# Kernel tuning notes

Measured on AMD Instinct MI355X. Metric: run time of the kernel, lower is better.

The kernel has to match this reference:

```python
import jax, jax.numpy as jnp
import numpy as np

QS = (0.25, 0.5, 0.75)


def _pool(inputs, maskb):
    """Masked summary-stats pooling: [B,S,F] -> [B, 7F+1]."""
    B, S, F = inputs.shape
    m = maskb[:, :, None].astype(inputs.dtype)          # [B,S,1]
    count = jnp.sum(m, axis=1)                          # [B,1]
    safe = jnp.maximum(count, 1.0)
    is_empty = count == 0                               # [B,1]
    mean = jnp.sum(inputs * m, axis=1) / safe           # [B,F]
    diffs = (inputs - mean[:, None, :]) * m
    var = jnp.sum(diffs * diffs, axis=1) / jnp.maximum(safe - 1.0, 1.0)
    std = jnp.sqrt(var)
    pinf = jnp.asarray(jnp.inf, inputs.dtype)
    mb3 = maskb[:, :, None]
    minv = jnp.min(jnp.where(mb3, inputs, pinf), axis=1)
    maxv = jnp.max(jnp.where(mb3, inputs, -pinf), axis=1)
    # nanquantile: sort with invalid entries pushed to the end (+inf),
    # then linear interpolation at q*(n-1) over the first n valid entries.
    xs = jnp.sort(jnp.where(mb3, inputs, pinf), axis=1)  # [B,S,F]
    n1 = jnp.maximum(count[:, 0] - 1.0, 0.0)             # [B]
    qv = []
    for q in QS:
        pos = q * n1                                     # [B]
        lo = jnp.clip(jnp.floor(pos).astype(jnp.int32), 0, S - 1)
        hi = jnp.clip(jnp.ceil(pos).astype(jnp.int32), 0, S - 1)
        frac = (pos - lo.astype(inputs.dtype))[:, None]  # [B,1]
        lov = jnp.take_along_axis(xs, jnp.broadcast_to(lo[:, None, None], (B, 1, F)), axis=1)[:, 0]
        hiv = jnp.take_along_axis(xs, jnp.broadcast_to(hi[:, None, None], (B, 1, F)), axis=1)[:, 0]
        qv.append(lov * (1.0 - frac) + hiv * frac)
    stats = [count, mean, qv[1], minv, maxv, std, qv[0], qv[2]]
    stats = [jnp.where(is_empty, jnp.zeros_like(s), s) for s in stats]
    return jnp.concatenate(stats, axis=1)                # [B, 7F+1]


def setup_inputs() -> dict:
    key = jax.random.key(0)
    ks = jax.random.split(key, 8)
    B, S, F = 256, 16384, 16
    D = 7 * F + 1  # 113
    inputs = jax.random.normal(ks[0], (B, S, F), dtype=jnp.float32)
    mask = jax.random.randint(ks[1], (B, S), 0, 2) > 0
    W1 = jax.random.normal(ks[2], (D, 16), dtype=jnp.float32) * 0.05
    b1 = jnp.zeros((16,), jnp.float32)
    W2 = jax.random.normal(ks[3], (16, 4), dtype=jnp.float32) * 0.05
    b2 = jnp.zeros((4,), jnp.float32)
    W3 = jax.random.normal(ks[4], (4, 1), dtype=jnp.float32) * 0.05
    b3 = jnp.zeros((1,), jnp.float32)
    return {"inputs": inputs, "mask": mask, "W1": W1, "b1": b1,
            "W2": W2, "b2": b2, "W3": W3, "b3": b3}


def reference(inputs, mask, W1, b1, W2, b2, W3, b3):
    pooled = _pool(inputs, mask)
    h = jax.nn.relu(pooled @ W1 + b1)   # dropout is identity in eval mode
    h = jax.nn.relu(h @ W2 + b2)
    return h @ W3 + b3                  # [B,1]
```

## Files before the change

### kernel.cpp

```cpp
#include <hip/hip_runtime.h>
#include <stdint.h>

#define B_DIM 256
#define S_DIM 16384
#define HALF_S 8192
#define D_DIM 113
#define NTH 1024
#define NIT 32
#define HDW 1024

__device__ __forceinline__ uint32_t enc_key(float v) {
    uint32_t u = __float_as_uint(v);
    uint32_t m = (uint32_t)((int32_t)u >> 31) | 0x80000000u;
    return u ^ m;
}
__device__ __forceinline__ float dec_key(uint32_t k) {
    uint32_t u = (k & 0x80000000u) ? (k ^ 0x80000000u) : ~k;
    return __uint_as_float(u);
}
__device__ __forceinline__ uint32_t umn(uint32_t a, uint32_t b) { return a < b ? a : b; }
__device__ __forceinline__ uint32_t umx(uint32_t a, uint32_t b) { return a > b ? a : b; }

__global__ __launch_bounds__(NTH, 8) void hist_kernel(
        const float* __restrict__ in, const unsigned char* __restrict__ mb,
        uint32_t* __restrict__ hws, float* __restrict__ psum,
        float* __restrict__ pssq, uint32_t* __restrict__ pkmin,
        uint32_t* __restrict__ pkmax, uint32_t* __restrict__ pn) {
    __shared__ uint32_t uni[16384];
    __shared__ float w_sum[16][16], w_ssq[16][16];
    __shared__ uint32_t w_kmin[16][16], w_kmax[16][16], w_cnt[16];
    __shared__ uint32_t s_det;

    const int t = threadIdx.x;
    const int b = blockIdx.x & 255;
    const int sh = blockIdx.x >> 8;
    const int c = t & 3;
    const float INFV = __uint_as_float(0x7F800000u);

    #pragma unroll
    for (int i = 0; i < 16; ++i) uni[i * NTH + t] = 0u;
    if (t == 0) s_det = 0u;
    {
        const uint32_t* mw32 = reinterpret_cast<const uint32_t*>(mb);
        uint32_t x = mw32[b * 1024 + t] & 0xFFFFFF00u;
        unsigned long long any = __ballot(x != 0);
        if ((t & 63) == 0 && any) atomicOr(&s_det, 1u);
    }
    __syncthreads();
    const size_t mstride = s_det ? (size_t)1 : (size_t)4;
    const unsigned char* __restrict__ mrow = mb + (size_t)b * S_DIM * mstride;

    const float4* __restrict__ base4 = reinterpret_cast<const float4*>(in)
        + (size_t)b * S_DIM * 4;

    float sumv[4] = {0.f, 0.f, 0.f, 0.f}, ssqv[4] = {0.f, 0.f, 0.f, 0.f};
    uint32_t kmn[4] = {~0u, ~0u, ~0u, ~0u}, kmx[4] = {0u, 0u, 0u, 0u};
    uint32_t cnt = 0;
    #pragma unroll 4
    for (int i = 0; i < NIT; ++i) {
        int s = sh * HALF_S + i * 256 + (t >> 2);
        float4 v = base4[(size_t)s * 4 + c];
        uint32_t m = mrow[(size_t)s * mstride] ? 1u : 0u;
        cnt += (c == 0) ? m : 0u;
        float vv[4] = {v.x, v.y, v.z, v.w};
        #pragma unroll
        for (int q = 0; q < 4; ++q) {
            float vh = m ? vv[q] : INFV;
            uint32_t key = enc_key(vh);
            kmn[q] = umn(kmn[q], key);
            kmx[q] = umx(kmx[q], m ? key : 0u);
            float vs = m ? vv[q] : 0.f;
            sumv[q] += vs;
            ssqv[q] = fmaf(vs, vs, ssqv[q]);
            if (m) {
                uint32_t bin = key >> 21;
                atomicAdd(&uni[((uint32_t)c * 4 + q) * HDW + (bin >> 1)],
                          (bin & 1) ? 65536u : 1u);
            }
        }
    }

    #pragma unroll
    for (int off = 32; off >= 4; off >>= 1) {
        #pragma unroll
        for (int q = 0; q < 4; ++q) {
            sumv[q] += __shfl_down(sumv[q], off);
            ssqv[q] += __shfl_down(ssqv[q], off);
            kmn[q] = umn(kmn[q], __shfl_down(kmn[q], off));
            kmx[q] = umx(kmx[q], __shfl_down(kmx[q], off));
        }
        cnt += __shfl_down(cnt, off);
    }
    {
        int w = t >> 6, lane = t & 63;
        if (lane < 4) {
            #pragma unroll
            for (int q = 0; q < 4; ++q) {
                w_sum[w][lane * 4 + q] = sumv[q];
                w_ssq[w][lane * 4 + q] = ssqv[q];
                w_kmin[w][lane * 4 + q] = kmn[q];
                w_kmax[w][lane * 4 + q] = kmx[q];
            }
            if (lane == 0) w_cnt[w] = cnt;
        }
    }
    __syncthreads();

    if (t < 16) {
        float s0 = 0.f, q0 = 0.f;
        uint32_t mnv = ~0u, mxv = 0u;
        for (int w = 0; w < 16; ++w) {
            s0 += w_sum[w][t]; q0 += w_ssq[w][t];
            mnv = umn(mnv, w_kmin[w][t]); mxv = umx(mxv, w_kmax[w][t]);
        }
        int bid = blockIdx.x;
        psum[bid * 16 + t] = s0; pssq[bid * 16 + t] = q0;
        pkmin[bid * 16 + t] = mnv; pkmax[bid * 16 + t] = mxv;
        if (t == 0) {
            uint32_t nn = 0;
            for (int w = 0; w < 16; ++w) nn += w_cnt[w];
            pn[bid] = nn;
        }
    }
    uint32_t* hb = hws + (size_t)blockIdx.x * 16384;
    #pragma unroll
    for (int i = 0; i < 16; ++i) hb[i * NTH + t] = uni[i * NTH + t];
}

__global__ __launch_bounds__(NTH, 4) void final_kernel(
        const uint32_t* __restrict__ hws, const float* __restrict__ psum,
        const float* __restrict__ pssq, const uint32_t* __restrict__ pkmin,
        const uint32_t* __restrict__ pkmax, const uint32_t* __restrict__ pn,
        const float* __restrict__ W1, const float* __restrict__ b1,
        const float* __restrict__ W2, const float* __restrict__ b2,
        const float* __restrict__ W3, const float* __restrict__ b3,
        float* __restrict__ out) {
    __shared__ uint32_t uni[16384];
    __shared__ uint32_t chunks[16][64];
    __shared__ float pool[128];
    __shared__ uint32_t s_nsh;

    const int t = threadIdx.x;
    const int b = blockIdx.x;

    const uint32_t* h0 = hws + (size_t)b * 16384;
    const uint32_t* h1 = hws + (size_t)(b + 256) * 16384;
    #pragma unroll
    for (int i = 0; i < 16; ++i) uni[i * NTH + t] = h0[i * NTH + t] + h1[i * NTH + t];
    if (t == 0) s_nsh = pn[b] + pn[b + 256];
    if (t < 128) pool[t] = 0.f;
    __syncthreads();
    const uint32_t n = s_nsh;

    if (n != 0) {
        if (t < 16) {
            float s0 = psum[b * 16 + t] + psum[(b + 256) * 16 + t];
            float q0 = pssq[b * 16 + t] + pssq[(b + 256) * 16 + t];
            uint32_t mnv = umn(pkmin[b * 16 + t], pkmin[(b + 256) * 16 + t]);
            uint32_t mxv = umx(pkmax[b * 16 + t], pkmax[(b + 256) * 16 + t]);
            float nf = (float)n;
            float mean = s0 / nf;
            float varn = q0 - s0 * s0 / nf;
            float denom = (float)(n >= 2 ? n - 1 : 1);
            float stdv = sqrtf(fmaxf(varn, 0.f) / denom);
            if (t == 0) pool[0] = nf;
            pool[1 + t] = mean;
            pool[33 + t] = dec_key(mnv);
            pool[49 + t] = dec_key(mxv);
            pool[65 + t] = stdv;
        }
        {
            int f = t >> 6, l = t & 63;
            uint32_t csum = 0;
            int base = f * HDW + l * 16;
            #pragma unroll
            for (int k = 0; k < 16; ++k) {
                uint32_t w = uni[base + ((k + l) & 15)];
                csum += (w & 0xFFFFu) + (w >> 16);
            }
            #pragma unroll
            for (int off = 1; off < 64; off <<= 1) {
                uint32_t o = __shfl_up(csum, off);
                if (l >= off) csum += o;
            }
            chunks[f][l] = csum;
        }
        __syncthreads();
        {
            int f = t >> 6, l = t & 63;
            if (l < 3) {
                float pos = 0.25f * (float)(l + 1) * (float)(n - 1);
                uint32_t r = (uint32_t)pos;
                int lo = 0, hi = 63;
                while (lo < hi) {
                    int mid = (lo + hi) >> 1;
                    if (chunks[f][mid] > r) hi = mid; else lo = mid + 1;
                }
                uint32_t acc = lo ? chunks[f][lo - 1] : 0u;
                uint32_t bin = (uint32_t)lo * 32u;
                for (;;) {
                    uint32_t w = uni[f * HDW + (bin >> 1)];
                    uint32_t h = (w >> ((bin & 1) * 16)) & 0xFFFFu;
                    if (acc + h > r) {
                        float pib = pos - (float)acc;
                        float vlo = dec_key(bin << 21);
                        float vhi = dec_key(umn((bin + 1) << 21, 0xFF7FFFFFu));
                        float qv = vlo + ((pib + 0.5f) / (float)h) * (vhi - vlo);
                        pool[(l == 0 ? 81 : (l == 1 ? 17 : 97)) + f] = qv;
                        break;
                    }
                    acc += h; ++bin;
                }
            }
        }
    }
    __syncthreads();

    if (t < 64) {
        float h = (t < 16) ? b1[t] : 0.f;
        for (int i = 0; i < D_DIM; ++i) {
            float pv = pool[i];
            if (t < 16) h += pv * W1[i * 16 + t];
        }
        if (t < 16) h = fmaxf(h, 0.f);
        float h2 = (t < 4) ? b2[t] : 0.f;
        #pragma unroll
        for (int j = 0; j < 16; ++j) {
            float hj = __shfl(h, j);
            if (t < 4) h2 += hj * W2[j * 4 + t];
        }
        if (t < 4) h2 = fmaxf(h2, 0.f);
        float o = 0.f;
        #pragma unroll
        for (int j = 0; j < 4; ++j) {
            float hj = __shfl(h2, j);
            o += hj * W3[j];
        }
        if (t == 0) out[b] = o + b3[0];
    }
}

extern "C" void kernel_launch(void* const* d_in, const int* in_sizes, int n_in,
                              void* d_out, int out_size, void* d_ws, size_t ws_size,
                              hipStream_t stream) {
    const float* inputs = (const float*)d_in[0];
    const unsigned char* mask = (const unsigned char*)d_in[1];
    const float* W1 = (const float*)d_in[2];
    const float* b1 = (const float*)d_in[3];
    const float* W2 = (const float*)d_in[4];
    const float* b2 = (const float*)d_in[5];
    const float* W3 = (const float*)d_in[6];
    const float* b3 = (const float*)d_in[7];
    float* out = (float*)d_out;

    char* w = (char*)d_ws;
    uint32_t* hws  = (uint32_t*)w;
    float*    psum = (float*)   (w + 33554432);
    float*    pssq = (float*)   (w + 33554432 + 32768);
    uint32_t* pkmn = (uint32_t*)(w + 33554432 + 65536);
    uint32_t* pkmx = (uint32_t*)(w + 33554432 + 98304);
    uint32_t* pn   = (uint32_t*)(w + 33554432 + 131072);

    hist_kernel<<<2 * B_DIM, NTH, 0, stream>>>(inputs, mask, hws, psum, pssq,
                                               pkmn, pkmx, pn);
    final_kernel<<<B_DIM, NTH, 0, stream>>>(hws, psum, pssq, pkmn, pkmx, pn,
                                            W1, b1, W2, b2, W3, b3, out);
}
```

Before: 115.7 us.

## Pre-pack mask into bitfield in separate kernels before histogram pass

Adds a detection kernel that decides whether the mask is stored as bytes or 4-byte bools, and a second kernel that packs the mask into 32-bit bitwords using ballot. The histogram kernel then loads 256 bitwords into LDS and builds a per-thread 32-bit mask register, replacing the strided per-element byte loads in its inner loop. In exchange it adds two extra launches and a full pass over the mask. The detection kernel runs as a single block reading serially, which may add latency.

```diff
diff --git a/kernel.cpp b/kernel.cpp
--- a/kernel.cpp
+++ b/kernel.cpp
@@ -21,15 +21,45 @@
 __device__ __forceinline__ uint32_t umn(uint32_t a, uint32_t b) { return a < b ? a : b; }
 __device__ __forceinline__ uint32_t umx(uint32_t a, uint32_t b) { return a > b ? a : b; }
 
+__global__ void detect_mask_kernel(const unsigned char* __restrict__ mb,
+                                   unsigned int* __restrict__ flag) {
+    __shared__ unsigned int acc[256];
+    int t = threadIdx.x;
+    unsigned int x = 0;
+    for (int i = 0; i < 256; ++i) {
+        int idx = t * 256 + i;
+        if ((idx & 3) != 0) x |= mb[idx];
+    }
+    acc[t] = x;
+    __syncthreads();
+    for (int off = 128; off; off >>= 1) {
+        if (t < off) acc[t] |= acc[t + off];
+        __syncthreads();
+    }
+    if (t == 0) *flag = (acc[0] != 0) ? 1u : 0u;
+}
+
+__global__ __launch_bounds__(256) void mask_bits_kernel(
+        const unsigned char* __restrict__ mb, const unsigned int* __restrict__ flag,
+        uint32_t* __restrict__ bits) {
+    size_t stride = (*flag) ? (size_t)1 : (size_t)4;
+    size_t e = (size_t)blockIdx.x * 256 + threadIdx.x;
+    uint32_t m = mb[e * stride] ? 1u : 0u;
+    unsigned long long bal = __ballot(m);
+    int lane = threadIdx.x & 63;
+    if (lane == 0) bits[e >> 5] = (uint32_t)bal;
+    else if (lane == 32) bits[e >> 5] = (uint32_t)(bal >> 32);
+}
+
 __global__ __launch_bounds__(NTH, 8) void hist_kernel(
-        const float* __restrict__ in, const unsigned char* __restrict__ mb,
+        const float* __restrict__ in, const uint32_t* __restrict__ bits,
         uint32_t* __restrict__ hws, float* __restrict__ psum,
         float* __restrict__ pssq, uint32_t* __restrict__ pkmin,
         uint32_t* __restrict__ pkmax, uint32_t* __restrict__ pn) {
     __shared__ uint32_t uni[16384];
+    __shared__ uint32_t ldsb[256];
     __shared__ float w_sum[16][16], w_ssq[16][16];
     __shared__ uint32_t w_kmin[16][16], w_kmax[16][16], w_cnt[16];
-    __shared__ uint32_t s_det;
 
     const int t = threadIdx.x;
     const int b = blockIdx.x & 255;
@@ -39,16 +69,16 @@
 
     #pragma unroll
     for (int i = 0; i < 16; ++i) uni[i * NTH + t] = 0u;
-    if (t == 0) s_det = 0u;
+    if (t < 256) ldsb[t] = bits[b * 512 + sh * 256 + t];
+    __syncthreads();
+
+    uint32_t mreg = 0u;
     {
-        const uint32_t* mw32 = reinterpret_cast<const uint32_t*>(mb);
-        uint32_t x = mw32[b * 1024 + t] & 0xFFFFFF00u;
-        unsigned long long any = __ballot(x != 0);
-        if ((t & 63) == 0 && any) atomicOr(&s_det, 1u);
-    }
-    __syncthreads();
-    const size_t mstride = s_det ? (size_t)1 : (size_t)4;
-    const unsigned char* __restrict__ mrow = mb + (size_t)b * S_DIM * mstride;
+        int word = t >> 7, sl = (t >> 2) & 31;
+        #pragma unroll
+        for (int i = 0; i < 32; ++i)
+            mreg |= ((ldsb[i * 8 + word] >> sl) & 1u) << i;
+    }
 
     const float4* __restrict__ base4 = reinterpret_cast<const float4*>(in)
         + (size_t)b * S_DIM * 4;
@@ -60,7 +90,7 @@
     for (int i = 0; i < NIT; ++i) {
         int s = sh * HALF_S + i * 256 + (t >> 2);
         float4 v = base4[(size_t)s * 4 + c];
-        uint32_t m = mrow[(size_t)s * mstride] ? 1u : 0u;
+        uint32_t m = (mreg >> i) & 1u;
         cnt += (c == 0) ? m : 0u;
         float vv[4] = {v.x, v.y, v.z, v.w};
         #pragma unroll
@@ -260,8 +290,12 @@
     uint32_t* pkmn = (uint32_t*)(w + 33554432 + 65536);
     uint32_t* pkmx = (uint32_t*)(w + 33554432 + 98304);
     uint32_t* pn   = (uint32_t*)(w + 33554432 + 131072);
-
-    hist_kernel<<<2 * B_DIM, NTH, 0, stream>>>(inputs, mask, hws, psum, pssq,
+    unsigned int* flag = (unsigned int*)(w + 33554432 + 135168);
+    uint32_t* bits = (uint32_t*)(w + 33554432 + 139264);
+
+    detect_mask_kernel<<<1, 256, 0, stream>>>(mask, flag);
+    mask_bits_kernel<<<(B_DIM * S_DIM) / 256, 256, 0, stream>>>(mask, flag, bits);
+    hist_kernel<<<2 * B_DIM, NTH, 0, stream>>>(inputs, bits, hws, psum, pssq,
                                                pkmn, pkmx, pn);
     final_kernel<<<B_DIM, NTH, 0, stream>>>(hws, psum, pssq, pkmn, pkmx, pn,
                                             W1, b1, W2, b2, W3, b3, out);
```

After: 153.3 us. +32.5%, slower.
